# Performance work log

Measured on AMD Instinct MI355X. Metric: run time of the kernel, lower is better.

Reference implementation:

```python
import jax, jax.numpy as jnp
import numpy as np

STEPS = 16      # max ICP iterations (module init arg `steps`)
TOL = 1e-6      # convergence tolerance (module init arg `tol`)


def _sqdist(a, b):
    # a: [B,N,3], b: [B,M,3] -> squared Euclidean distances [B,N,M] via GEMM
    a2 = jnp.sum(a * a, axis=-1)            # [B,N]
    b2 = jnp.sum(b * b, axis=-1)            # [B,M]
    ab = jnp.einsum('bnd,bmd->bnm', a, b)   # [B,N,M]
    return jnp.maximum(a2[..., :, None] + b2[..., None, :] - 2.0 * ab, 0.0)


def _kabsch(src, tgt):
    # Rigid transform (R, t) minimizing ||R*src + t - tgt|| via 3x3 SVD (svdtf)
    cs = src.mean(axis=-2, keepdims=True)   # [B,1,3]
    ct = tgt.mean(axis=-2, keepdims=True)
    H = jnp.einsum('bni,bnj->bij', src - cs, tgt - ct)  # [B,3,3]
    U, S, Vt = jnp.linalg.svd(H)
    V = jnp.swapaxes(Vt, -1, -2)
    Ut = jnp.swapaxes(U, -1, -2)
    d = jnp.linalg.det(V @ Ut)              # [B], reflection fix
    D = (jnp.zeros_like(H)
         .at[..., 0, 0].set(1.0)
         .at[..., 1, 1].set(1.0)
         .at[..., 2, 2].set(d))
    R = V @ D @ Ut                          # [B,3,3]
    t = ct[..., 0, :] - jnp.einsum('bij,bj->bi', R, cs[..., 0, :])  # [B,3]
    return R, t


def _icp(source, target):
    B = source.shape[0]

    def step(carry, _):
        temporal, errlast, done = carry
        d2 = _sqdist(temporal, target)                      # [B,N,M]
        knnidx = jnp.argmin(d2, axis=-1)                    # [B,N] 1-NN indices
        knnd2 = jnp.take_along_axis(d2, knnidx[..., None], axis=-1)[..., 0]
        errnew = jnp.sqrt(knnd2).mean(axis=-1)              # [B]
        # early-exit: once all batch errors converged, freeze state (emulates break)
        done = done | jnp.all(jnp.abs(errnew - errlast) < TOL)
        knntgt = jnp.take_along_axis(target, knnidx[..., None], axis=-2)  # [B,N,3]
        R, t = _kabsch(temporal, knntgt)
        new_temporal = jnp.einsum('bij,bnj->bni', R, temporal) + t[:, None, :]
        temporal = jnp.where(done, temporal, new_temporal)
        errlast = jnp.where(done, errlast, errnew)
        return (temporal, errlast, done), None

    init = (source, jnp.zeros((B,), source.dtype), jnp.array(False))
    (temporal, _, _), _ = jax.lax.scan(step, init, None, length=STEPS)
    # final transform from original source to aligned cloud (svdtf(source, temporal))
    R, t = _kabsch(source, temporal)
    return jnp.concatenate([R, t[..., None]], axis=-1)    # [B,3,4] = [R | t]


def setup_inputs() -> dict:
    key = jax.random.key(0)
    k1, k2 = jax.random.split(key)
    source = jax.random.normal(k1, (4, 4096, 3), dtype=jnp.float32)
    target = jax.random.normal(k2, (4, 4096, 3), dtype=jnp.float32)
    return {"source": source, "target": target}


def reference(source, target):
    return _icp(source, target)
```

## Files before the change

### kernel.cpp

```cpp
#include <hip/hip_runtime.h>

#define BATCH   4
#define NPTS    4096
#define MPTS    4096
#define NSTEPS  16
#define ICP_TOL 1e-6f

#define TPB        512
#define NBLOCKS    256
#define BLK_PER_B  64

#define ACC_OFF 0
#define CNT_OFF 65536
#define MST_OFF 69632
#define ZERO_DWORDS (69632/4)


__device__ inline void normalize3d(double v[3]) {
    double n = sqrt(v[0]*v[0] + v[1]*v[1] + v[2]*v[2]);
    double inv = (n > 1e-300) ? 1.0 / n : 0.0;
    v[0] *= inv; v[1] *= inv; v[2] *= inv;
}

__device__ inline void cross3d(const double a[3], const double b[3], double c[3]) {
    c[0] = a[1]*b[2] - a[2]*b[1];
    c[1] = a[2]*b[0] - a[0]*b[2];
    c[2] = a[0]*b[1] - a[1]*b[0];
}

__device__ inline void eigvec_from_product(const double K[3][3], double la, double lb, double v[3]) {
    double A[3][3], Bm[3][3], C[3][3];
    #pragma unroll
    for (int i = 0; i < 3; i++)
        #pragma unroll
        for (int j = 0; j < 3; j++) {
            A[i][j]  = K[i][j] - ((i == j) ? la : 0.0);
            Bm[i][j] = K[i][j] - ((i == j) ? lb : 0.0);
        }
    #pragma unroll
    for (int i = 0; i < 3; i++)
        #pragma unroll
        for (int j = 0; j < 3; j++) {
            double s = 0.0;
            #pragma unroll
            for (int k = 0; k < 3; k++) s += A[i][k] * Bm[k][j];
            C[i][j] = s;
        }
    int best = 0; double bn = -1.0;
    #pragma unroll
    for (int c = 0; c < 3; c++) {
        double n2 = C[0][c]*C[0][c] + C[1][c]*C[1][c] + C[2][c]*C[2][c];
        if (n2 > bn) { bn = n2; best = c; }
    }
    if (bn > 1e-280) {
        double inv = 1.0 / sqrt(bn);
        v[0] = C[0][best]*inv; v[1] = C[1][best]*inv; v[2] = C[2][best]*inv;
    } else {
        v[0] = 1.0; v[1] = 0.0; v[2] = 0.0;
    }
}

__device__ inline void kabsch_from_sums(const double S[16], double R[3][3], double t[3]) {
    const double inv_n = 1.0 / (double)NPTS;
    double cs[3] = { S[0]*inv_n, S[1]*inv_n, S[2]*inv_n };
    double ct[3] = { S[3]*inv_n, S[4]*inv_n, S[5]*inv_n };
    double H[3][3];
    #pragma unroll
    for (int i = 0; i < 3; i++)
        #pragma unroll
        for (int j = 0; j < 3; j++)
            H[i][j] = S[6 + 3*i + j] - S[i]*S[3 + j]*inv_n;

    double K[3][3];
    #pragma unroll
    for (int i = 0; i < 3; i++)
        #pragma unroll
        for (int j = 0; j < 3; j++) {
            double s = 0.0;
            #pragma unroll
            for (int k = 0; k < 3; k++) s += H[k][i]*H[k][j];
            K[i][j] = s;
        }

    double q = (K[0][0] + K[1][1] + K[2][2]) / 3.0;
    double p1 = K[0][1]*K[0][1] + K[0][2]*K[0][2] + K[1][2]*K[1][2];
    double a00 = K[0][0]-q, a11 = K[1][1]-q, a22 = K[2][2]-q;
    double p2 = a00*a00 + a11*a11 + a22*a22 + 2.0*p1;
    double p = sqrt(p2 / 6.0);
    double l1, l2, l3;
    if (p < 1e-150) {
        l1 = l2 = l3 = q;
    } else {
        double ip = 1.0 / p;
        double b00 = a00*ip, b01 = K[0][1]*ip, b02 = K[0][2]*ip;
        double b11 = a11*ip, b12 = K[1][2]*ip, b22 = a22*ip;
        double detB = b00*(b11*b22 - b12*b12)
                    - b01*(b01*b22 - b12*b02)
                    + b02*(b01*b12 - b11*b02);
        double r = 0.5 * detB;
        r = r < -1.0 ? -1.0 : (r > 1.0 ? 1.0 : r);
        float phi = acosf((float)r) * (1.0f/3.0f);
        l1 = q + 2.0*p*(double)cosf(phi);
        l3 = q + 2.0*p*(double)cosf(phi + 2.0943951f);
        l2 = 3.0*q - l1 - l3;
    }

    double v1[3], v2[3], v3[3];
    eigvec_from_product(K, l2, l3, v1);
    eigvec_from_product(K, l1, l3, v2);
    double d12 = v1[0]*v2[0] + v1[1]*v2[1] + v1[2]*v2[2];
    #pragma unroll
    for (int i = 0; i < 3; i++) v2[i] -= d12*v1[i];
    normalize3d(v2);
    cross3d(v1, v2, v3);

    double u1[3], u2[3], u3[3];
    #pragma unroll
    for (int i = 0; i < 3; i++) u1[i] = H[i][0]*v1[0] + H[i][1]*v1[1] + H[i][2]*v1[2];
    normalize3d(u1);
    #pragma unroll
    for (int i = 0; i < 3; i++) u2[i] = H[i][0]*v2[0] + H[i][1]*v2[1] + H[i][2]*v2[2];
    double du = u1[0]*u2[0] + u1[1]*u2[1] + u1[2]*u2[2];
    #pragma unroll
    for (int i = 0; i < 3; i++) u2[i] -= du*u1[i];
    normalize3d(u2);
    cross3d(u1, u2, u3);

    #pragma unroll
    for (int i = 0; i < 3; i++)
        #pragma unroll
        for (int j = 0; j < 3; j++)
            R[i][j] = v1[i]*u1[j] + v2[i]*u2[j] + v3[i]*u3[j];
    #pragma unroll
    for (int i = 0; i < 3; i++)
        t[i] = ct[i] - (R[i][0]*cs[0] + R[i][1]*cs[1] + R[i][2]*cs[2]);
}


__global__ void k_init(unsigned int* __restrict__ wsz) {
    int i = blockIdx.x * blockDim.x + threadIdx.x;
    if (i < ZERO_DWORDS) wsz[i] = 0u;
}

__global__ __launch_bounds__(TPB)
void k_icp(const float* __restrict__ src, const float* __restrict__ tgt,
           double* __restrict__ accD, unsigned int* __restrict__ cntU,
           float* __restrict__ MstF) {
    __shared__ float4 t4c[MPTS];
    __shared__ double pmem[8][16];
    __shared__ double Ssh[16];

    const int bid  = blockIdx.x;
    const int b    = bid >> 6;
    const int lb   = bid & (BLK_PER_B - 1);
    const int tid  = threadIdx.x;
    const int w    = tid >> 6;
    const int lane = tid & 63;

    const float* tgb = tgt + (size_t)b * MPTS * 3;
    const float* spb = src + ((size_t)b * NPTS + lb * 64 + w * 8) * 3;

    for (int i = tid; i < MPTS; i += TPB) {
        float x = tgb[3*i], y = tgb[3*i+1], z = tgb[3*i+2];
        t4c[i] = make_float4(x, y, z, 0.5f*(x*x + y*y + z*z));
    }

    float px[8], py[8], pz[8];
    #pragma unroll
    for (int k = 0; k < 8; k++) {
        px[k] = spb[3*k+0]; py[k] = spb[3*k+1]; pz[k] = spb[3*k+2];
    }
    float m00=1.f,m01=0.f,m02=0.f, m10=0.f,m11=1.f,m12=0.f, m20=0.f,m21=0.f,m22=1.f;
    float mt0=0.f,mt1=0.f,mt2=0.f;
    __syncthreads();

    for (int s = 0; s < NSTEPS; ++s) {
        float bs[8]; int bm[8];
        #pragma unroll
        for (int k = 0; k < 8; k++) { bs[k] = 1e30f; bm[k] = 0; }

        #pragma unroll 4
        for (int j = 0; j < MPTS/64; ++j) {
            int ml = (j << 6) | lane;
            float4 T = t4c[ml];
            #pragma unroll
            for (int k = 0; k < 8; k++) {
                float sc = __fmaf_rn(-px[k], T.x, T.w);
                sc = __fmaf_rn(-py[k], T.y, sc);
                sc = __fmaf_rn(-pz[k], T.z, sc);
                if (sc < bs[k]) { bs[k] = sc; bm[k] = ml; }
            }
        }
        #pragma unroll
        for (int off = 32; off >= 1; off >>= 1) {
            #pragma unroll
            for (int k = 0; k < 8; k++) {
                float os = __shfl_xor(bs[k], off);
                int   om = __shfl_xor(bm[k], off);
                if (os < bs[k] || (os == bs[k] && om < bm[k])) { bs[k] = os; bm[k] = om; }
            }
        }
        if (lane == 0) {
            double acc[16];
            #pragma unroll
            for (int i = 0; i < 16; i++) acc[i] = 0.0;
            #pragma unroll
            for (int k = 0; k < 8; k++) {
                float4 q4 = t4c[bm[k]];
                float a2 = px[k]*px[k] + py[k]*py[k] + pz[k]*pz[k];
                float d2 = fmaxf(a2 + 2.0f*bs[k], 0.0f);
                double pxd = px[k], pyd = py[k], pzd = pz[k];
                double qxd = q4.x, qyd = q4.y, qzd = q4.z;
                acc[0] += pxd;  acc[1] += pyd;  acc[2] += pzd;
                acc[3] += qxd;  acc[4] += qyd;  acc[5] += qzd;
                acc[6] += pxd*qxd;  acc[7]  += pxd*qyd;  acc[8]  += pxd*qzd;
                acc[9] += pyd*qxd;  acc[10] += pyd*qyd;  acc[11] += pyd*qzd;
                acc[12]+= pzd*qxd;  acc[13] += pzd*qyd;  acc[14] += pzd*qzd;
                acc[15]+= (double)sqrtf(d2);
            }
            #pragma unroll
            for (int i = 0; i < 16; i++) pmem[w][i] = acc[i];
        }
        __syncthreads();

        const int slot = (s * BATCH + b) * 16;
        if (tid < 16) {
            double v = pmem[0][tid] + pmem[1][tid] + pmem[2][tid] + pmem[3][tid]
                     + pmem[4][tid] + pmem[5][tid] + pmem[6][tid] + pmem[7][tid];
            unsafeAtomicAdd(&accD[(size_t)(slot + tid) * 8], v);
        }
        asm volatile("s_waitcnt vmcnt(0)" ::: "memory");
        if (tid == 0) {
            unsigned int* cp = &cntU[(size_t)(s * BATCH + b) * 16];
            __hip_atomic_fetch_add(cp, 1u, __ATOMIC_RELAXED, __HIP_MEMORY_SCOPE_AGENT);
            while (__hip_atomic_load(cp, __ATOMIC_ACQUIRE, __HIP_MEMORY_SCOPE_AGENT) < BLK_PER_B)
                __builtin_amdgcn_s_sleep(16);
        }
        if (tid < 16)
            Ssh[tid] = __hip_atomic_load(&accD[(size_t)(slot + tid) * 8],
                                         __ATOMIC_RELAXED, __HIP_MEMORY_SCOPE_AGENT);
        __syncthreads();

        double S[16];
        #pragma unroll
        for (int i = 0; i < 16; i++) S[i] = Ssh[i];
        float errnew = (float)(S[15] * (1.0 / (double)NPTS));
        double R[3][3], t[3];
        kabsch_from_sums(S, R, t);
        float r00=(float)R[0][0], r01=(float)R[0][1], r02=(float)R[0][2];
        float r10=(float)R[1][0], r11=(float)R[1][1], r12=(float)R[1][2];
        float r20=(float)R[2][0], r21=(float)R[2][1], r22=(float)R[2][2];
        float t0=(float)t[0], t1=(float)t[1], t2=(float)t[2];

        #pragma unroll
        for (int k = 0; k < 8; k++) {
            float x = px[k], y = py[k], z = pz[k];
            px[k] = r00*x + r01*y + r02*z + t0;
            py[k] = r10*x + r11*y + r12*z + t1;
            pz[k] = r20*x + r21*y + r22*z + t2;
        }
        float n00 = r00*m00 + r01*m10 + r02*m20;
        float n01 = r00*m01 + r01*m11 + r02*m21;
        float n02 = r00*m02 + r01*m12 + r02*m22;
        float n10 = r10*m00 + r11*m10 + r12*m20;
        float n11 = r10*m01 + r11*m11 + r12*m21;
        float n12 = r10*m02 + r11*m12 + r12*m22;
        float n20 = r20*m00 + r21*m10 + r22*m20;
        float n21 = r20*m01 + r21*m11 + r22*m21;
        float n22 = r20*m02 + r21*m12 + r22*m22;
        float nt0 = r00*mt0 + r01*mt1 + r02*mt2 + t0;
        float nt1 = r10*mt0 + r11*mt1 + r12*mt2 + t1;
        float nt2 = r20*mt0 + r21*mt1 + r22*mt2 + t2;
        m00=n00; m01=n01; m02=n02; m10=n10; m11=n11; m12=n12;
        m20=n20; m21=n21; m22=n22; mt0=nt0; mt1=nt1; mt2=nt2;

        if (lb == 0 && tid == 0) {
            float* o = MstF + (size_t)(s * BATCH + b) * 16;
            o[0] = errnew;
            o[1] = m00; o[2] = m01; o[3] = m02;
            o[4] = m10; o[5] = m11; o[6] = m12;
            o[7] = m20; o[8] = m21; o[9] = m22;
            o[10] = mt0; o[11] = mt1; o[12] = mt2;
        }
    }
}

__global__ void k_final(const float* __restrict__ MstF, float* __restrict__ out) {
    const int lane = threadIdx.x;
    float ep0 = 0.f, ep1 = 0.f, ep2 = 0.f, ep3 = 0.f;
    int sel = NSTEPS - 1;
    bool ident = false;
    bool found = false;
    for (int s = 0; s < NSTEPS && !found; ++s) {
        float e0 = MstF[(s*4+0)*16], e1 = MstF[(s*4+1)*16];
        float e2 = MstF[(s*4+2)*16], e3 = MstF[(s*4+3)*16];
        if (fabsf(e0-ep0) < ICP_TOL && fabsf(e1-ep1) < ICP_TOL &&
            fabsf(e2-ep2) < ICP_TOL && fabsf(e3-ep3) < ICP_TOL) {
            found = true;
            if (s == 0) ident = true; else sel = s - 1;
        } else {
            ep0 = e0; ep1 = e1; ep2 = e2; ep3 = e3;
        }
    }
    if (lane < BATCH) {
        float* o = out + lane * 12;
        if (ident) {
            o[0]=1.f; o[1]=0.f; o[2]=0.f; o[3]=0.f;
            o[4]=0.f; o[5]=1.f; o[6]=0.f; o[7]=0.f;
            o[8]=0.f; o[9]=0.f; o[10]=1.f; o[11]=0.f;
        } else {
            const float* m = MstF + (size_t)(sel*4 + lane) * 16;
            o[0]=m[1];  o[1]=m[2];  o[2]=m[3];  o[3]=m[10];
            o[4]=m[4];  o[5]=m[5];  o[6]=m[6];  o[7]=m[11];
            o[8]=m[7];  o[9]=m[8];  o[10]=m[9]; o[11]=m[12];
        }
    }
}


extern "C" void kernel_launch(void* const* d_in, const int* in_sizes, int n_in,
                              void* d_out, int out_size, void* d_ws, size_t ws_size,
                              hipStream_t stream) {
    const float* src = (const float*)d_in[0];
    const float* tgt = (const float*)d_in[1];
    float* out = (float*)d_out;

    char* ws = (char*)d_ws;
    double*       accD = (double*)(ws + ACC_OFF);
    unsigned int* cntU = (unsigned int*)(ws + CNT_OFF);
    float*        MstF = (float*)(ws + MST_OFF);

    k_init<<<dim3((ZERO_DWORDS + 255)/256), dim3(256), 0, stream>>>((unsigned int*)ws);
    k_icp<<<dim3(NBLOCKS), dim3(TPB), 0, stream>>>(src, tgt, accD, cntU, MstF);
    k_final<<<dim3(1), dim3(64), 0, stream>>>(MstF, out);
}
```

Before: 442.6 us.

## Double block count, use packed FMA over SoA target, single-wave Kabsch

Doubles the grid to 512 blocks with 4 source points per wave instead of 8, so more CUs take part in the cooperative per-step reduction. The target cloud moves to structure-of-arrays in shared memory, and scores are computed two candidates at a time with v_pk_fma_f32 plus a branchless min/argmin. Only wave 0 computes the double-precision Kabsch solve and shares R and t through LDS, the spin-wait sleep is shortened, and a trailing barrier is added. The risks are more blocks in the grid-wide spin barrier, which needs all 512 blocks co-resident, plus extra syncs per step and possible tie-breaking differences in argmin order.

```diff
diff --git a/kernel.cpp b/kernel.cpp
--- a/kernel.cpp
+++ b/kernel.cpp
@@ -7,13 +7,15 @@
 #define ICP_TOL 1e-6f
 
 #define TPB        512
-#define NBLOCKS    256
-#define BLK_PER_B  64
+#define NBLOCKS    512
+#define BLK_PER_B  128
 
 #define ACC_OFF 0
 #define CNT_OFF 65536
 #define MST_OFF 69632
 #define ZERO_DWORDS (69632/4)
+
+typedef float v2f __attribute__((ext_vector_type(2)));
 
 
 __device__ inline void normalize3d(double v[3]) {
@@ -142,59 +144,81 @@
     if (i < ZERO_DWORDS) wsz[i] = 0u;
 }
 
-__global__ __launch_bounds__(TPB)
+__global__ __launch_bounds__(TPB, 4)
 void k_icp(const float* __restrict__ src, const float* __restrict__ tgt,
            double* __restrict__ accD, unsigned int* __restrict__ cntU,
            float* __restrict__ MstF) {
-    __shared__ float4 t4c[MPTS];
+    __shared__ __align__(16) float Xs[MPTS];
+    __shared__ __align__(16) float Ys[MPTS];
+    __shared__ __align__(16) float Zs[MPTS];
+    __shared__ __align__(16) float Ws[MPTS];
     __shared__ double pmem[8][16];
     __shared__ double Ssh[16];
+    __shared__ float  Rsh[13];
 
     const int bid  = blockIdx.x;
-    const int b    = bid >> 6;
+    const int b    = bid >> 7;
     const int lb   = bid & (BLK_PER_B - 1);
     const int tid  = threadIdx.x;
     const int w    = tid >> 6;
     const int lane = tid & 63;
 
     const float* tgb = tgt + (size_t)b * MPTS * 3;
-    const float* spb = src + ((size_t)b * NPTS + lb * 64 + w * 8) * 3;
+    const float* spb = src + ((size_t)b * NPTS + lb * 32 + w * 4) * 3;
 
     for (int i = tid; i < MPTS; i += TPB) {
         float x = tgb[3*i], y = tgb[3*i+1], z = tgb[3*i+2];
-        t4c[i] = make_float4(x, y, z, 0.5f*(x*x + y*y + z*z));
-    }
-
-    float px[8], py[8], pz[8];
-    #pragma unroll
-    for (int k = 0; k < 8; k++) {
+        Xs[i] = x; Ys[i] = y; Zs[i] = z;
+        Ws[i] = 0.5f*(x*x + y*y + z*z);
+    }
+
+    float px[4], py[4], pz[4];
+    #pragma unroll
+    for (int k = 0; k < 4; k++) {
         px[k] = spb[3*k+0]; py[k] = spb[3*k+1]; pz[k] = spb[3*k+2];
     }
     float m00=1.f,m01=0.f,m02=0.f, m10=0.f,m11=1.f,m12=0.f, m20=0.f,m21=0.f,m22=1.f;
     float mt0=0.f,mt1=0.f,mt2=0.f;
     __syncthreads();
 
+    const v2f* Xv = (const v2f*)Xs;
+    const v2f* Yv = (const v2f*)Ys;
+    const v2f* Zv = (const v2f*)Zs;
+    const v2f* Wv = (const v2f*)Ws;
+
     for (int s = 0; s < NSTEPS; ++s) {
-        float bs[8]; int bm[8];
-        #pragma unroll
-        for (int k = 0; k < 8; k++) { bs[k] = 1e30f; bm[k] = 0; }
+        v2f nx[4], ny[4], nz[4];
+        #pragma unroll
+        for (int k = 0; k < 4; k++) {
+            nx[k] = (v2f){-px[k], -px[k]};
+            ny[k] = (v2f){-py[k], -py[k]};
+            nz[k] = (v2f){-pz[k], -pz[k]};
+        }
+        float bs[4]; int bm[4];
+        #pragma unroll
+        for (int k = 0; k < 4; k++) { bs[k] = 1e30f; bm[k] = 0; }
 
         #pragma unroll 4
-        for (int j = 0; j < MPTS/64; ++j) {
-            int ml = (j << 6) | lane;
-            float4 T = t4c[ml];
-            #pragma unroll
-            for (int k = 0; k < 8; k++) {
-                float sc = __fmaf_rn(-px[k], T.x, T.w);
-                sc = __fmaf_rn(-py[k], T.y, sc);
-                sc = __fmaf_rn(-pz[k], T.z, sc);
-                if (sc < bs[k]) { bs[k] = sc; bm[k] = ml; }
+        for (int j = 0; j < (MPTS/2)/64; ++j) {
+            int q = (j << 6) | lane;
+            v2f Xp = Xv[q], Yp = Yv[q], Zp = Zv[q], Wp = Wv[q];
+            #pragma unroll
+            for (int k = 0; k < 4; k++) {
+                v2f f0, f1, f2;
+                asm("v_pk_fma_f32 %0, %1, %2, %3" : "=v"(f0) : "v"(nx[k]), "v"(Xp), "v"(Wp));
+                asm("v_pk_fma_f32 %0, %1, %2, %3" : "=v"(f1) : "v"(ny[k]), "v"(Yp), "v"(f0));
+                asm("v_pk_fma_f32 %0, %1, %2, %3" : "=v"(f2) : "v"(nz[k]), "v"(Zp), "v"(f1));
+                float lo = f2.x, hi = f2.y;
+                float bsn = fminf(fminf(lo, hi), bs[k]);
+                int ip = (q << 1) | ((hi < lo) ? 1 : 0);
+                bm[k] = (bsn < bs[k]) ? ip : bm[k];
+                bs[k] = bsn;
             }
         }
         #pragma unroll
         for (int off = 32; off >= 1; off >>= 1) {
             #pragma unroll
-            for (int k = 0; k < 8; k++) {
+            for (int k = 0; k < 4; k++) {
                 float os = __shfl_xor(bs[k], off);
                 int   om = __shfl_xor(bm[k], off);
                 if (os < bs[k] || (os == bs[k] && om < bm[k])) { bs[k] = os; bm[k] = om; }
@@ -205,12 +229,13 @@
             #pragma unroll
             for (int i = 0; i < 16; i++) acc[i] = 0.0;
             #pragma unroll
-            for (int k = 0; k < 8; k++) {
-                float4 q4 = t4c[bm[k]];
+            for (int k = 0; k < 4; k++) {
+                int mm = bm[k];
+                float qx = Xs[mm], qy = Ys[mm], qz = Zs[mm];
                 float a2 = px[k]*px[k] + py[k]*py[k] + pz[k]*pz[k];
                 float d2 = fmaxf(a2 + 2.0f*bs[k], 0.0f);
                 double pxd = px[k], pyd = py[k], pzd = pz[k];
-                double qxd = q4.x, qyd = q4.y, qzd = q4.z;
+                double qxd = qx, qyd = qy, qzd = qz;
                 acc[0] += pxd;  acc[1] += pyd;  acc[2] += pzd;
                 acc[3] += qxd;  acc[4] += qyd;  acc[5] += qzd;
                 acc[6] += pxd*qxd;  acc[7]  += pxd*qyd;  acc[8]  += pxd*qzd;
@@ -234,26 +259,36 @@
             unsigned int* cp = &cntU[(size_t)(s * BATCH + b) * 16];
             __hip_atomic_fetch_add(cp, 1u, __ATOMIC_RELAXED, __HIP_MEMORY_SCOPE_AGENT);
             while (__hip_atomic_load(cp, __ATOMIC_ACQUIRE, __HIP_MEMORY_SCOPE_AGENT) < BLK_PER_B)
-                __builtin_amdgcn_s_sleep(16);
+                __builtin_amdgcn_s_sleep(2);
         }
         if (tid < 16)
             Ssh[tid] = __hip_atomic_load(&accD[(size_t)(slot + tid) * 8],
                                          __ATOMIC_RELAXED, __HIP_MEMORY_SCOPE_AGENT);
         __syncthreads();
 
-        double S[16];
-        #pragma unroll
-        for (int i = 0; i < 16; i++) S[i] = Ssh[i];
-        float errnew = (float)(S[15] * (1.0 / (double)NPTS));
-        double R[3][3], t[3];
-        kabsch_from_sums(S, R, t);
-        float r00=(float)R[0][0], r01=(float)R[0][1], r02=(float)R[0][2];
-        float r10=(float)R[1][0], r11=(float)R[1][1], r12=(float)R[1][2];
-        float r20=(float)R[2][0], r21=(float)R[2][1], r22=(float)R[2][2];
-        float t0=(float)t[0], t1=(float)t[1], t2=(float)t[2];
-
-        #pragma unroll
-        for (int k = 0; k < 8; k++) {
+        if (w == 0) {
+            double S[16];
+            #pragma unroll
+            for (int i = 0; i < 16; i++) S[i] = Ssh[i];
+            double R[3][3], t[3];
+            kabsch_from_sums(S, R, t);
+            if (lane == 0) {
+                Rsh[0]=(float)R[0][0]; Rsh[1]=(float)R[0][1]; Rsh[2]=(float)R[0][2];
+                Rsh[3]=(float)R[1][0]; Rsh[4]=(float)R[1][1]; Rsh[5]=(float)R[1][2];
+                Rsh[6]=(float)R[2][0]; Rsh[7]=(float)R[2][1]; Rsh[8]=(float)R[2][2];
+                Rsh[9]=(float)t[0];    Rsh[10]=(float)t[1];   Rsh[11]=(float)t[2];
+                Rsh[12]=(float)(S[15] * (1.0 / (double)NPTS));
+            }
+        }
+        __syncthreads();
+
+        const float r00=Rsh[0], r01=Rsh[1], r02=Rsh[2];
+        const float r10=Rsh[3], r11=Rsh[4], r12=Rsh[5];
+        const float r20=Rsh[6], r21=Rsh[7], r22=Rsh[8];
+        const float t0=Rsh[9], t1=Rsh[10], t2=Rsh[11];
+
+        #pragma unroll
+        for (int k = 0; k < 4; k++) {
             float x = px[k], y = py[k], z = pz[k];
             px[k] = r00*x + r01*y + r02*z + t0;
             py[k] = r10*x + r11*y + r12*z + t1;
@@ -276,12 +311,13 @@
 
         if (lb == 0 && tid == 0) {
             float* o = MstF + (size_t)(s * BATCH + b) * 16;
-            o[0] = errnew;
+            o[0] = Rsh[12];
             o[1] = m00; o[2] = m01; o[3] = m02;
             o[4] = m10; o[5] = m11; o[6] = m12;
             o[7] = m20; o[8] = m21; o[9] = m22;
             o[10] = mt0; o[11] = mt1; o[12] = mt2;
         }
+        __syncthreads();
     }
 }
 
```

Result: slower. 478.4 us (+8.1%).
